# Optimization experiments

Measured on AMD Instinct MI355X. Metric: run time of the kernel, lower is better.

## Reference

```python
import jax, jax.numpy as jnp
import numpy as np

NGRAM_N = 4

def ngram_repeat_mask(toks, n):
    # toks: [B, S] int32. Mark positions j..j+n-1 for every ngram starting at
    # j (j in range(S-n)) that already appeared at an earlier start position.
    B, S = toks.shape
    P = S - n  # number of ngram start positions, matching range(len(x)-n)
    win = jnp.arange(P)[:, None] + jnp.arange(n)[None, :]  # [P, n]
    G = toks[:, win]                                        # [B, P, n]
    eq = (G[:, :, None, :] == G[:, None, :, :]).all(-1)     # [B, P, P]
    prev = jnp.tril(jnp.ones((P, P), dtype=bool), k=-1)     # j' < j
    repeated = (eq & prev[None]).any(-1)                    # [B, P]
    # dilate forward over the ngram window: mask[j:j+n] = 1 if repeated[j]
    shifted = jnp.stack([jnp.pad(repeated, ((0, 0), (k, S - P - k)))
                         for k in range(n)], axis=0)        # [n, B, S]
    return shifted.any(0).astype(jnp.float32)               # [B, S]

def setup_inputs() -> dict:
    key = jax.random.key(0)
    B, V, S = 8, 32000, 512
    pred = jax.random.normal(key, (B, V, S), dtype=jnp.float32)
    return {"pred": pred}

def reference(pred):
    # pred: [B, V, S] logits
    B = pred.shape[0]
    pred_toks = jnp.argmax(pred, axis=1)                    # [B, S] int
    pred_lprobs_full = jax.nn.log_softmax(pred, axis=1)     # [B, V, S]
    # gather log-prob of the argmax token at each position -> [B, S]
    pred_lprobs = jnp.take_along_axis(pred_lprobs_full, pred_toks[:, None, :], axis=1)[:, 0, :]
    one_minus_probs = jnp.clip(1.0 - jnp.exp(pred_lprobs), 1e-20, None)
    mask = ngram_repeat_mask(pred_toks, NGRAM_N)            # [B, S] float
    loss = (-jnp.log(one_minus_probs) * mask).sum() / B
    return loss
```

## Files before the change

### kernel.cpp

```cpp
#include <hip/hip_runtime.h>
#include <math.h>

#define BB 8
#define VV 32000
#define SS 512
#define NCHUNK 125
#define CHUNK 256
#define NCOL (BB * SS)
#define NGRAM 4
#define PP (SS - NGRAM)

__global__ __launch_bounds__(256) void colstats_kernel(const float* __restrict__ pred,
                                                       float* __restrict__ pmax,
                                                       float* __restrict__ psum,
                                                       int* __restrict__ pidx) {
    const int bid = blockIdx.x;
    const int b   = bid / NCHUNK;
    const int c   = bid - b * NCHUNK;
    const int tid = threadIdx.x;
    const int vo  = tid >> 7;
    const int s   = (tid & 127) << 2;
    const int v0  = c * CHUNK;

    float m0 = -INFINITY, m1 = -INFINITY, m2 = -INFINITY, m3 = -INFINITY;
    float a0 = 0.f, a1 = 0.f, a2 = 0.f, a3 = 0.f;
    int   i0 = 0, i1 = 0, i2 = 0, i3 = 0;

    const float L2E = 1.4426950408889634f;
    const float* ptr = pred + ((size_t)(b * VV + v0 + vo)) * SS + s;
    int v = v0 + vo;
#pragma unroll 8
    for (int k = 0; k < CHUNK / 2; ++k) {
        const float4 x = *(const float4*)ptr;
        ptr += 2 * SS;
        a0 += exp2f(x.x * L2E);
        a1 += exp2f(x.y * L2E);
        a2 += exp2f(x.z * L2E);
        a3 += exp2f(x.w * L2E);
        if (x.x > m0) { m0 = x.x; i0 = v; }
        if (x.y > m1) { m1 = x.y; i1 = v; }
        if (x.z > m2) { m2 = x.z; i2 = v; }
        if (x.w > m3) { m3 = x.w; i3 = v; }
        v += 2;
    }

    __shared__ float smax[256][4];
    __shared__ float ssum[256][4];
    __shared__ int   sidx[256][4];
    smax[tid][0] = m0; smax[tid][1] = m1; smax[tid][2] = m2; smax[tid][3] = m3;
    ssum[tid][0] = a0; ssum[tid][1] = a1; ssum[tid][2] = a2; ssum[tid][3] = a3;
    sidx[tid][0] = i0; sidx[tid][1] = i1; sidx[tid][2] = i2; sidx[tid][3] = i3;
    __syncthreads();

    if (tid < 128) {
        const int o = tid + 128;
        float m[4]  = {smax[tid][0], smax[tid][1], smax[tid][2], smax[tid][3]};
        float a[4]  = {ssum[tid][0], ssum[tid][1], ssum[tid][2], ssum[tid][3]};
        int   ix[4] = {sidx[tid][0], sidx[tid][1], sidx[tid][2], sidx[tid][3]};
#pragma unroll
        for (int j = 0; j < 4; ++j) {
            const float om = smax[o][j];
            const int   oi = sidx[o][j];
            a[j] += ssum[o][j];
            if (om > m[j] || (om == m[j] && oi < ix[j])) { m[j] = om; ix[j] = oi; }
        }
        const size_t ob = (size_t)c * NCOL + (size_t)b * SS + (size_t)s;
#pragma unroll
        for (int j = 0; j < 4; ++j) {
            pmax[ob + j] = m[j];
            psum[ob + j] = a[j];
            pidx[ob + j] = ix[j];
        }
    }
}

__global__ __launch_bounds__(256) void finalize_kernel(const float* __restrict__ pmax,
                                                       const float* __restrict__ psum,
                                                       const int* __restrict__ pidx,
                                                       int* __restrict__ toks,
                                                       float* __restrict__ pen,
                                                       float* __restrict__ out) {
    const int tid  = threadIdx.x;
    const int col  = blockIdx.x * 64 + (tid >> 2);
    const int part = tid & 3;

    if (blockIdx.x == 0 && tid == 0) out[0] = 0.0f;

    const int cbeg = part * 32;
    int cend = cbeg + 32; if (cend > NCHUNK) cend = NCHUNK;

    float m = -INFINITY, sum = 0.f;
    int   idx = 0x7fffffff;
    for (int c = cbeg; c < cend; ++c) {
        const int off = c * NCOL + col;
        const float cm = pmax[off];
        const int   ci = pidx[off];
        sum += psum[off];
        if (cm > m || (cm == m && ci < idx)) { m = cm; idx = ci; }
    }

    __shared__ float sm[256], ss[256];
    __shared__ int   si[256];
    sm[tid] = m; ss[tid] = sum; si[tid] = idx;
    __syncthreads();

    if (part == 0) {
#pragma unroll
        for (int j = 1; j < 4; ++j) {
            const float om = sm[tid + j];
            const int   oi = si[tid + j];
            sum += ss[tid + j];
            if (om > m || (om == m && oi < idx)) { m = om; idx = oi; }
        }
        const float lprob = m - logf(sum);
        const float p = expf(lprob);
        float om1 = 1.0f - p;
        if (om1 < 1e-20f) om1 = 1e-20f;
        pen[col]  = -logf(om1);
        toks[col] = idx;
    }
}

__global__ __launch_bounds__(256) void mask_loss_kernel(const int* __restrict__ toks,
                                                        const float* __restrict__ pen,
                                                        float* __restrict__ out) {
    const int b   = blockIdx.x;
    const int tid = threadIdx.x;
    __shared__ int tk[SS];
    __shared__ int rep[SS];
    for (int i = tid; i < SS; i += 256) { tk[i] = toks[b * SS + i]; rep[i] = 0; }
    __syncthreads();

    for (int i = tid; i < PP; i += 256) {
        const int c0 = tk[i], c1 = tk[i + 1], c2 = tk[i + 2], c3 = tk[i + 3];
        int r = 0;
        for (int j = 0; j < i; ++j) {
            if (tk[j] == c0 && tk[j + 1] == c1 && tk[j + 2] == c2 && tk[j + 3] == c3) {
                r = 1; break;
            }
        }
        rep[i] = r;
    }
    __syncthreads();

    float local = 0.f;
    for (int s = tid; s < SS; s += 256) {
        int msk = 0;
#pragma unroll
        for (int k = 0; k < NGRAM; ++k) {
            const int i = s - k;
            if (i >= 0 && i < PP && rep[i]) msk = 1;
        }
        if (msk) local += pen[b * SS + s];
    }

    for (int off = 32; off > 0; off >>= 1) local += __shfl_down(local, off, 64);
    __shared__ float wsum[4];
    const int lane = tid & 63, wid = tid >> 6;
    if (lane == 0) wsum[wid] = local;
    __syncthreads();
    if (tid == 0) {
        float t = wsum[0] + wsum[1] + wsum[2] + wsum[3];
        atomicAdd(out, t * (1.0f / (float)BB));
    }
}

extern "C" void kernel_launch(void* const* d_in, const int* in_sizes, int n_in,
                              void* d_out, int out_size, void* d_ws, size_t ws_size,
                              hipStream_t stream) {
    const float* pred = (const float*)d_in[0];
    float* out = (float*)d_out;
    char* ws = (char*)d_ws;

    const size_t partN = (size_t)NCHUNK * NCOL;
    float* pmax = (float*)ws;
    float* psum = (float*)(ws + partN * 4);
    int*   pidx = (int*)  (ws + partN * 8);
    int*   toks = (int*)  (ws + partN * 12);
    float* pen  = (float*)(ws + partN * 12 + NCOL * 4);

    colstats_kernel<<<BB * NCHUNK, 256, 0, stream>>>(pred, pmax, psum, pidx);
    finalize_kernel<<<NCOL / 64, 256, 0, stream>>>(pmax, psum, pidx, toks, pen, out);
    mask_loss_kernel<<<BB, 256, 0, stream>>>(toks, pen, out);
}
```

Before: 755.9 us.

## Fuse finalize into mask kernel and use nontemporal loads with native exp2

The separate finalize and mask/loss kernels are merged into one kernel per batch row with 512 threads, so tokens and penalties stay in shared memory instead of going through global memory. The output zeroing moves to a tiny separate kernel. The column-stats kernel switches to nontemporal vector loads and the hardware exp2 builtin. The fused kernel runs only 8 blocks, each serially reducing 125 chunks per column, so it cuts a launch and some traffic but parallelises the partial reduction poorly.

Result: faster. 715.9 us (-5.3%).

```diff
diff --git a/kernel.cpp b/kernel.cpp
--- a/kernel.cpp
+++ b/kernel.cpp
@@ -9,6 +9,9 @@
 #define NCOL (BB * SS)
 #define NGRAM 4
 #define PP (SS - NGRAM)
+#define NREAL (BB * NCHUNK)
+
+typedef float vfloat4 __attribute__((ext_vector_type(4)));
 
 __global__ __launch_bounds__(256) void colstats_kernel(const float* __restrict__ pred,
                                                        float* __restrict__ pmax,
@@ -27,16 +30,16 @@
     int   i0 = 0, i1 = 0, i2 = 0, i3 = 0;
 
     const float L2E = 1.4426950408889634f;
-    const float* ptr = pred + ((size_t)(b * VV + v0 + vo)) * SS + s;
+    const vfloat4* ptr = (const vfloat4*)(pred + ((size_t)(b * VV + v0 + vo)) * SS + s);
     int v = v0 + vo;
 #pragma unroll 8
     for (int k = 0; k < CHUNK / 2; ++k) {
-        const float4 x = *(const float4*)ptr;
-        ptr += 2 * SS;
-        a0 += exp2f(x.x * L2E);
-        a1 += exp2f(x.y * L2E);
-        a2 += exp2f(x.z * L2E);
-        a3 += exp2f(x.w * L2E);
+        const vfloat4 x = __builtin_nontemporal_load(ptr);
+        ptr += (2 * SS) / 4;
+        a0 += __builtin_amdgcn_exp2f(x.x * L2E);
+        a1 += __builtin_amdgcn_exp2f(x.y * L2E);
+        a2 += __builtin_amdgcn_exp2f(x.z * L2E);
+        a3 += __builtin_amdgcn_exp2f(x.w * L2E);
         if (x.x > m0) { m0 = x.x; i0 = v; }
         if (x.y > m1) { m1 = x.y; i1 = v; }
         if (x.z > m2) { m2 = x.z; i2 = v; }
@@ -74,93 +77,71 @@
     }
 }
 
-__global__ __launch_bounds__(256) void finalize_kernel(const float* __restrict__ pmax,
-                                                       const float* __restrict__ psum,
-                                                       const int* __restrict__ pidx,
-                                                       int* __restrict__ toks,
-                                                       float* __restrict__ pen,
-                                                       float* __restrict__ out) {
-    const int tid  = threadIdx.x;
-    const int col  = blockIdx.x * 64 + (tid >> 2);
-    const int part = tid & 3;
+__global__ void zero_kernel(float* out) { out[0] = 0.0f; }
 
-    if (blockIdx.x == 0 && tid == 0) out[0] = 0.0f;
-
-    const int cbeg = part * 32;
-    int cend = cbeg + 32; if (cend > NCHUNK) cend = NCHUNK;
+__global__ __launch_bounds__(512) void finalize_mask_kernel(const float* __restrict__ pmax,
+                                                            const float* __restrict__ psum,
+                                                            const int* __restrict__ pidx,
+                                                            float* __restrict__ out) {
+    const int b   = blockIdx.x;
+    const int tid = threadIdx.x;
+    const int col = b * SS + tid;
 
     float m = -INFINITY, sum = 0.f;
     int   idx = 0x7fffffff;
-    for (int c = cbeg; c < cend; ++c) {
+#pragma unroll 5
+    for (int c = 0; c < NCHUNK; ++c) {
         const int off = c * NCOL + col;
         const float cm = pmax[off];
         const int   ci = pidx[off];
         sum += psum[off];
         if (cm > m || (cm == m && ci < idx)) { m = cm; idx = ci; }
     }
+    const float lprob = m - logf(sum);
+    const float p = expf(lprob);
+    float om1 = 1.0f - p;
+    if (om1 < 1e-20f) om1 = 1e-20f;
 
-    __shared__ float sm[256], ss[256];
-    __shared__ int   si[256];
-    sm[tid] = m; ss[tid] = sum; si[tid] = idx;
+    __shared__ int   tk[SS];
+    __shared__ int   rep[SS];
+    __shared__ float pn[SS];
+    tk[tid]  = idx;
+    pn[tid]  = -logf(om1);
+    rep[tid] = 0;
     __syncthreads();
 
-    if (part == 0) {
-#pragma unroll
-        for (int j = 1; j < 4; ++j) {
-            const float om = sm[tid + j];
-            const int   oi = si[tid + j];
-            sum += ss[tid + j];
-            if (om > m || (om == m && oi < idx)) { m = om; idx = oi; }
-        }
-        const float lprob = m - logf(sum);
-        const float p = expf(lprob);
-        float om1 = 1.0f - p;
-        if (om1 < 1e-20f) om1 = 1e-20f;
-        pen[col]  = -logf(om1);
-        toks[col] = idx;
-    }
-}
-
-__global__ __launch_bounds__(256) void mask_loss_kernel(const int* __restrict__ toks,
-                                                        const float* __restrict__ pen,
-                                                        float* __restrict__ out) {
-    const int b   = blockIdx.x;
-    const int tid = threadIdx.x;
-    __shared__ int tk[SS];
-    __shared__ int rep[SS];
-    for (int i = tid; i < SS; i += 256) { tk[i] = toks[b * SS + i]; rep[i] = 0; }
-    __syncthreads();
-
-    for (int i = tid; i < PP; i += 256) {
-        const int c0 = tk[i], c1 = tk[i + 1], c2 = tk[i + 2], c3 = tk[i + 3];
+    if (tid < PP) {
+        const int c0 = tk[tid], c1 = tk[tid + 1], c2 = tk[tid + 2], c3 = tk[tid + 3];
         int r = 0;
-        for (int j = 0; j < i; ++j) {
+        for (int j = 0; j < tid; ++j) {
             if (tk[j] == c0 && tk[j + 1] == c1 && tk[j + 2] == c2 && tk[j + 3] == c3) {
                 r = 1; break;
             }
         }
-        rep[i] = r;
+        rep[tid] = r;
     }
     __syncthreads();
 
     float local = 0.f;
-    for (int s = tid; s < SS; s += 256) {
+    {
         int msk = 0;
 #pragma unroll
         for (int k = 0; k < NGRAM; ++k) {
-            const int i = s - k;
+            const int i = tid - k;
             if (i >= 0 && i < PP && rep[i]) msk = 1;
         }
-        if (msk) local += pen[b * SS + s];
+        if (msk) local += pn[tid];
     }
 
     for (int off = 32; off > 0; off >>= 1) local += __shfl_down(local, off, 64);
-    __shared__ float wsum[4];
+    __shared__ float wsum[8];
     const int lane = tid & 63, wid = tid >> 6;
     if (lane == 0) wsum[wid] = local;
     __syncthreads();
     if (tid == 0) {
-        float t = wsum[0] + wsum[1] + wsum[2] + wsum[3];
+        float t = 0.f;
+#pragma unroll
+        for (int w = 0; w < 8; ++w) t += wsum[w];
         atomicAdd(out, t * (1.0f / (float)BB));
     }
 }
@@ -176,10 +157,8 @@
     float* pmax = (float*)ws;
     float* psum = (float*)(ws + partN * 4);
     int*   pidx = (int*)  (ws + partN * 8);
-    int*   toks = (int*)  (ws + partN * 12);
-    float* pen  = (float*)(ws + partN * 12 + NCOL * 4);
 
-    colstats_kernel<<<BB * NCHUNK, 256, 0, stream>>>(pred, pmax, psum, pidx);
-    finalize_kernel<<<NCOL / 64, 256, 0, stream>>>(pmax, psum, pidx, toks, pen, out);
-    mask_loss_kernel<<<BB, 256, 0, stream>>>(toks, pen, out);
+    colstats_kernel<<<NREAL, 256, 0, stream>>>(pred, pmax, psum, pidx);
+    zero_kernel<<<1, 1, 0, stream>>>(out);
+    finalize_mask_kernel<<<BB, 512, 0, stream>>>(pmax, psum, pidx, out);
 }
```
